# Performance work log

Hardware: AMD Instinct MI355X
Metric: run time of the kernel (lower is better)

## Reference

```python
import jax, jax.numpy as jnp
import numpy as np

N, E = 20000, 320000
H = 4            # heads per layer
C_IN, C_HID, C_OUT = 128, 64, 64
NEG_SLOPE = 0.2  # PyG GATConv default leaky_relu slope


def setup_inputs() -> dict:
    key = jax.random.key(0)
    ks = jax.random.split(key, 16)
    p = lambda k, shape: jax.random.normal(k, shape, jnp.float32) * 0.1
    return {
        "x": jax.random.normal(ks[0], (N, C_IN), jnp.float32),
        "edge_index": jax.random.randint(ks[1], (2, E), 0, N),
        # layer 0: in C_IN -> H*C_HID (concat)
        "W0": p(ks[2], (C_IN, H * C_HID)),
        "as0": p(ks[3], (H, C_HID)),
        "ad0": p(ks[4], (H, C_HID)),
        "b0": jnp.zeros((H * C_HID,), jnp.float32),
        # layer 1: in H*C_HID -> H*C_HID (concat)
        "W1": p(ks[5], (H * C_HID, H * C_HID)),
        "as1": p(ks[6], (H, C_HID)),
        "ad1": p(ks[7], (H, C_HID)),
        "b1": jnp.zeros((H * C_HID,), jnp.float32),
        # output layer: in H*C_HID -> C_OUT (mean over heads, concat=False)
        "W2": p(ks[8], (H * C_HID, H * C_OUT)),
        "as2": p(ks[9], (H, C_OUT)),
        "ad2": p(ks[10], (H, C_OUT)),
        "b2": jnp.zeros((C_OUT,), jnp.float32),
    }


def _gat_layer(x, src, dst, W, a_src, a_dst, b, concat):
    """PyG GATConv (eval mode): gather -> edge attention -> segment softmax -> scatter."""
    n = x.shape[0]
    h = (x @ W).reshape(n, H, -1)                      # [N, H, C]
    e_src = (h * a_src).sum(-1)                        # [N, H]
    e_dst = (h * a_dst).sum(-1)                        # [N, H]
    logits = jax.nn.leaky_relu(e_src[src] + e_dst[dst], NEG_SLOPE)   # [E', H]
    m = jax.lax.stop_gradient(jax.ops.segment_max(logits, dst, num_segments=n))
    ex = jnp.exp(logits - m[dst])
    denom = jax.ops.segment_sum(ex, dst, num_segments=n)
    alpha = ex / denom[dst]                            # [E', H] segment softmax per dst node
    out = jax.ops.segment_sum(h[src] * alpha[:, :, None], dst, num_segments=n)  # [N, H, C]
    out = out.reshape(n, -1) if concat else out.mean(axis=1)
    return out + b, alpha


def reference(x, edge_index, W0, as0, ad0, b0, W1, as1, ad1, b1, W2, as2, ad2, b2):
    n = x.shape[0]
    loops = jnp.arange(n, dtype=edge_index.dtype)      # GATConv adds self-loops
    src = jnp.concatenate([edge_index[0], loops])
    dst = jnp.concatenate([edge_index[1], loops])
    h, a0 = _gat_layer(x, src, dst, W0, as0, ad0, b0, True)
    h = jax.nn.elu(h)
    h, a1 = _gat_layer(h, src, dst, W1, as1, ad1, b1, True)
    h = jax.nn.elu(h)
    out, a2 = _gat_layer(h, src, dst, W2, as2, ad2, b2, False)
    return out, a0, a1, a2
```

## Files before the change

kernel.cpp:

```cpp
#include <hip/hip_runtime.h>
#include <hip/hip_bf16.h>
#include <math.h>

#define HCOLS 256
#define NHEAD 4
#define CDIM  64
#define NEG_SLOPE 0.2f

typedef __attribute__((ext_vector_type(8))) short bf16x8;
typedef __attribute__((ext_vector_type(4))) float f32x4;

__device__ __forceinline__ float leaky(float v) { return v > 0.f ? v : v * NEG_SLOPE; }
__device__ __forceinline__ float readlane_f(float v, int l) {
    return __uint_as_float(__builtin_amdgcn_readlane(__float_as_uint(v), l));
}
__device__ __forceinline__ unsigned short f2bf(float f) {
    unsigned u = __float_as_uint(f);
    u += 0x7fff + ((u >> 16) & 1);
    return (unsigned short)(u >> 16);
}
__device__ __forceinline__ float bf2f(unsigned short b) {
    return __uint_as_float(((unsigned)b) << 16);
}

__global__ void deg_kernel(const int* __restrict__ ei, int* __restrict__ deg,
                           int E, int Ep) {
    int e = blockIdx.x * 256 + threadIdx.x;
    if (e >= Ep) return;
    int d = (e < E) ? ei[E + e] : (e - E);
    atomicAdd(&deg[d], 1);
}

__global__ void scan_kernel(const int* __restrict__ deg, int* __restrict__ rowptr,
                            int* __restrict__ cursor, int n) {
    __shared__ int tmp[1024];
    __shared__ int carry_s;
    int tid = threadIdx.x;
    if (tid == 0) carry_s = 0;
    __syncthreads();
    for (int base = 0; base < n; base += 1024) {
        int i = base + tid;
        int v = (i < n) ? deg[i] : 0;
        tmp[tid] = v;
        __syncthreads();
        for (int off = 1; off < 1024; off <<= 1) {
            int t = (tid >= off) ? tmp[tid - off] : 0;
            __syncthreads();
            tmp[tid] += t;
            __syncthreads();
        }
        int excl = carry_s + tmp[tid] - v;
        if (i < n) { rowptr[i] = excl; cursor[i] = excl; }
        __syncthreads();
        if (tid == 1023) carry_s += tmp[1023];
        __syncthreads();
    }
    if (tid == 0) rowptr[n] = carry_s;
}

__global__ void fill_kernel(const int* __restrict__ ei, int* __restrict__ cursor,
                            int* __restrict__ eidx, int E, int Ep) {
    int e = blockIdx.x * 256 + threadIdx.x;
    if (e >= Ep) return;
    int d = (e < E) ? ei[E + e] : (e - E);
    int pos = atomicAdd(&cursor[d], 1);
    eidx[pos] = e;
}

__global__ void wconv_kernel(const float* __restrict__ W, unsigned short* __restrict__ Wt, int K) {
    __shared__ float t[32][33];
    int bx = blockIdx.x;
    int by = blockIdx.y;
    int tx = threadIdx.x & 31, ty = threadIdx.x >> 5;
#pragma unroll
    for (int i = 0; i < 32; i += 8)
        t[ty + i][tx] = W[(by * 32 + ty + i) * HCOLS + bx * 32 + tx];
    __syncthreads();
#pragma unroll
    for (int i = 0; i < 32; i += 8)
        Wt[(size_t)(bx * 32 + ty + i) * K + by * 32 + tx] = f2bf(t[tx][ty + i]);
}

template <int K, bool SRC_F32>
__global__ void gemm_kernel(const void* __restrict__ Xv, const unsigned short* __restrict__ Wt,
                            unsigned short* __restrict__ Hout,
                            const float* __restrict__ As, const float* __restrict__ Ad,
                            float* __restrict__ esrc, float* __restrict__ edst,
                            int n) {
    constexpr int LDK = K + 16;
    __shared__ __align__(16) unsigned short a_sh[32 * LDK];
    int row0 = blockIdx.x * 32;
    int tid = threadIdx.x;

    constexpr int CH = 32 * K / 8;
    for (int c = tid; c < CH; c += 256) {
        int r = c / (K / 8), kc = c % (K / 8);
        int row = row0 + r;
        uint4 pack;
        if (row < n) {
            if (SRC_F32) {
                const float* X = (const float*)Xv;
                float4 f0 = *reinterpret_cast<const float4*>(&X[(size_t)row * K + kc * 8]);
                float4 f1 = *reinterpret_cast<const float4*>(&X[(size_t)row * K + kc * 8 + 4]);
                pack.x = f2bf(f0.x) | ((unsigned)f2bf(f0.y) << 16);
                pack.y = f2bf(f0.z) | ((unsigned)f2bf(f0.w) << 16);
                pack.z = f2bf(f1.x) | ((unsigned)f2bf(f1.y) << 16);
                pack.w = f2bf(f1.z) | ((unsigned)f2bf(f1.w) << 16);
            } else {
                const uint4* X = (const uint4*)Xv;
                pack = X[((size_t)row * K + kc * 8) / 8];
            }
        } else {
            pack = make_uint4(0, 0, 0, 0);
        }
        *reinterpret_cast<uint4*>(&a_sh[r * LDK + kc * 8]) = pack;
    }
    __syncthreads();

    int lane = tid & 63;
    int w = tid >> 6;
    int lr = lane & 15;
    int lk = (lane >> 4) * 8;

    f32x4 acc[2][4];
#pragma unroll
    for (int m = 0; m < 2; ++m)
#pragma unroll
        for (int nf = 0; nf < 4; ++nf) acc[m][nf] = (f32x4){0.f, 0.f, 0.f, 0.f};

    const unsigned short* wt = Wt + (size_t)(w * 64) * K;
#pragma unroll
    for (int ks = 0; ks < K / 32; ++ks) {
        bf16x8 a[2], b[4];
#pragma unroll
        for (int m = 0; m < 2; ++m)
            a[m] = *reinterpret_cast<const bf16x8*>(&a_sh[(16 * m + lr) * LDK + ks * 32 + lk]);
#pragma unroll
        for (int nf = 0; nf < 4; ++nf)
            b[nf] = *reinterpret_cast<const bf16x8*>(&wt[(size_t)(16 * nf + lr) * K + ks * 32 + lk]);
#pragma unroll
        for (int m = 0; m < 2; ++m)
#pragma unroll
            for (int nf = 0; nf < 4; ++nf)
                acc[m][nf] = __builtin_amdgcn_mfma_f32_16x16x32_bf16(a[m], b[nf], acc[m][nf], 0, 0, 0);
    }

    float as_v[4], ad_v[4];
#pragma unroll
    for (int nf = 0; nf < 4; ++nf) {
        as_v[nf] = As[w * 64 + 16 * nf + lr];
        ad_v[nf] = Ad[w * 64 + 16 * nf + lr];
    }
#pragma unroll
    for (int m = 0; m < 2; ++m) {
#pragma unroll
        for (int j = 0; j < 4; ++j) {
            int row_g = row0 + 16 * m + (lane >> 4) * 4 + j;
            bool ok = row_g < n;
#pragma unroll
            for (int nf = 0; nf < 4; ++nf) {
                if (ok) Hout[(size_t)row_g * HCOLS + w * 64 + 16 * nf + lr] = f2bf(acc[m][nf][j]);
            }
            float ps = acc[m][0][j] * as_v[0] + acc[m][1][j] * as_v[1] +
                       acc[m][2][j] * as_v[2] + acc[m][3][j] * as_v[3];
            float pd = acc[m][0][j] * ad_v[0] + acc[m][1][j] * ad_v[1] +
                       acc[m][2][j] * ad_v[2] + acc[m][3][j] * ad_v[3];
#pragma unroll
            for (int off = 1; off < 16; off <<= 1) {
                ps += __shfl_xor(ps, off, 64);
                pd += __shfl_xor(pd, off, 64);
            }
            if (lr == 0 && ok) {
                esrc[row_g * NHEAD + w] = ps;
                edst[row_g * NHEAD + w] = pd;
            }
        }
    }
}

template <int MODE>
__global__ void attn_agg_kernel(const unsigned short* __restrict__ h,
                                const float* __restrict__ esrc,
                                const float* __restrict__ edst,
                                const int* __restrict__ ei,
                                const int* __restrict__ rowptr,
                                const int* __restrict__ eidx,
                                const float* __restrict__ bias,
                                float* __restrict__ alpha,
                                void* __restrict__ xout,
                                int n, int E) {
    int wave = threadIdx.x >> 6;
    int lane = threadIdx.x & 63;
    int node = blockIdx.x * 4 + wave;
    if (node >= n) return;
    int s0 = rowptr[node], s1 = rowptr[node + 1];
    int deg = s1 - s0;
    float4 ed = *reinterpret_cast<const float4*>(&edst[node * NHEAD]);

    int i0 = s0 + lane;
    bool valid = i0 < s1;
    int e0 = 0, sv = 0;
    float4 lg0 = make_float4(-3.4e38f, -3.4e38f, -3.4e38f, -3.4e38f);
    if (valid) {
        e0 = eidx[i0];
        sv = (e0 < E) ? ei[e0] : (e0 - E);
        float4 es = *reinterpret_cast<const float4*>(&esrc[sv * NHEAD]);
        lg0.x = leaky(es.x + ed.x);
        lg0.y = leaky(es.y + ed.y);
        lg0.z = leaky(es.z + ed.z);
        lg0.w = leaky(es.w + ed.w);
    }
    float4 mx = lg0;
    for (int i = i0 + 64; i < s1; i += 64) {
        int e = eidx[i];
        int s = (e < E) ? ei[e] : (e - E);
        float4 es = *reinterpret_cast<const float4*>(&esrc[s * NHEAD]);
        mx.x = fmaxf(mx.x, leaky(es.x + ed.x));
        mx.y = fmaxf(mx.y, leaky(es.y + ed.y));
        mx.z = fmaxf(mx.z, leaky(es.z + ed.z));
        mx.w = fmaxf(mx.w, leaky(es.w + ed.w));
    }
#pragma unroll
    for (int off = 32; off; off >>= 1) {
        mx.x = fmaxf(mx.x, __shfl_xor(mx.x, off, 64));
        mx.y = fmaxf(mx.y, __shfl_xor(mx.y, off, 64));
        mx.z = fmaxf(mx.z, __shfl_xor(mx.z, off, 64));
        mx.w = fmaxf(mx.w, __shfl_xor(mx.w, off, 64));
    }
    float4 ex0 = make_float4(0.f, 0.f, 0.f, 0.f);
    if (valid) {
        ex0.x = __expf(lg0.x - mx.x);
        ex0.y = __expf(lg0.y - mx.y);
        ex0.z = __expf(lg0.z - mx.z);
        ex0.w = __expf(lg0.w - mx.w);
    }
    float4 sm = ex0;
    for (int i = i0 + 64; i < s1; i += 64) {
        int e = eidx[i];
        int s = (e < E) ? ei[e] : (e - E);
        float4 es = *reinterpret_cast<const float4*>(&esrc[s * NHEAD]);
        sm.x += __expf(leaky(es.x + ed.x) - mx.x);
        sm.y += __expf(leaky(es.y + ed.y) - mx.y);
        sm.z += __expf(leaky(es.z + ed.z) - mx.z);
        sm.w += __expf(leaky(es.w + ed.w) - mx.w);
    }
#pragma unroll
    for (int off = 32; off; off >>= 1) {
        sm.x += __shfl_xor(sm.x, off, 64);
        sm.y += __shfl_xor(sm.y, off, 64);
        sm.z += __shfl_xor(sm.z, off, 64);
        sm.w += __shfl_xor(sm.w, off, 64);
    }
    float4 inv = make_float4(1.f / sm.x, 1.f / sm.y, 1.f / sm.z, 1.f / sm.w);
    float4 al = make_float4(ex0.x * inv.x, ex0.y * inv.y, ex0.z * inv.z, ex0.w * inv.w);
    if (valid) *reinterpret_cast<float4*>(&alpha[(size_t)e0 * NHEAD]) = al;
    for (int i = i0 + 64; i < s1; i += 64) {
        int e = eidx[i];
        int s = (e < E) ? ei[e] : (e - E);
        float4 es = *reinterpret_cast<const float4*>(&esrc[s * NHEAD]);
        float4 av;
        av.x = __expf(leaky(es.x + ed.x) - mx.x) * inv.x;
        av.y = __expf(leaky(es.y + ed.y) - mx.y) * inv.y;
        av.z = __expf(leaky(es.z + ed.z) - mx.z) * inv.z;
        av.w = __expf(leaky(es.w + ed.w) - mx.w) * inv.w;
        *reinterpret_cast<float4*>(&alpha[(size_t)e * NHEAD]) = av;
    }
    bool big = deg > 64;
    if (big) __threadfence();

    int head = lane >> 4;
    float4 acc = make_float4(0.f, 0.f, 0.f, 0.f);
    int m = deg < 64 ? deg : 64;
    for (int j = 0; j < m; ++j) {
        int s = __builtin_amdgcn_readlane(sv, j);
        float a0v = readlane_f(al.x, j);
        float a1v = readlane_f(al.y, j);
        float a2v = readlane_f(al.z, j);
        float a3v = readlane_f(al.w, j);
        float a = (head & 2) ? ((head & 1) ? a3v : a2v) : ((head & 1) ? a1v : a0v);
        ushort4 hv = *reinterpret_cast<const ushort4*>(&h[(size_t)s * HCOLS + (lane << 2)]);
        acc.x = fmaf(a, bf2f(hv.x), acc.x);
        acc.y = fmaf(a, bf2f(hv.y), acc.y);
        acc.z = fmaf(a, bf2f(hv.z), acc.z);
        acc.w = fmaf(a, bf2f(hv.w), acc.w);
    }
    if (big) {
        for (int i = s0 + 64; i < s1; ++i) {
            int e = eidx[i];
            int s = (e < E) ? ei[e] : (e - E);
            float4 av = *reinterpret_cast<const float4*>(&alpha[(size_t)e * NHEAD]);
            float a = (head & 2) ? ((head & 1) ? av.w : av.z) : ((head & 1) ? av.y : av.x);
            ushort4 hv = *reinterpret_cast<const ushort4*>(&h[(size_t)s * HCOLS + (lane << 2)]);
            acc.x = fmaf(a, bf2f(hv.x), acc.x);
            acc.y = fmaf(a, bf2f(hv.y), acc.y);
            acc.z = fmaf(a, bf2f(hv.z), acc.z);
            acc.w = fmaf(a, bf2f(hv.w), acc.w);
        }
    }
    if (MODE == 0) {
        float4 bv = *reinterpret_cast<const float4*>(&bias[lane << 2]);
        float4 v;
        v.x = acc.x + bv.x; v.y = acc.y + bv.y; v.z = acc.z + bv.z; v.w = acc.w + bv.w;
        v.x = v.x > 0.f ? v.x : expm1f(v.x);
        v.y = v.y > 0.f ? v.y : expm1f(v.y);
        v.z = v.z > 0.f ? v.z : expm1f(v.z);
        v.w = v.w > 0.f ? v.w : expm1f(v.w);
        ushort4 o;
        o.x = f2bf(v.x); o.y = f2bf(v.y); o.z = f2bf(v.z); o.w = f2bf(v.w);
        *reinterpret_cast<ushort4*>(&((unsigned short*)xout)[(size_t)node * HCOLS + (lane << 2)]) = o;
    } else {
        acc.x += __shfl_xor(acc.x, 16, 64); acc.x += __shfl_xor(acc.x, 32, 64);
        acc.y += __shfl_xor(acc.y, 16, 64); acc.y += __shfl_xor(acc.y, 32, 64);
        acc.z += __shfl_xor(acc.z, 16, 64); acc.z += __shfl_xor(acc.z, 32, 64);
        acc.w += __shfl_xor(acc.w, 16, 64); acc.w += __shfl_xor(acc.w, 32, 64);
        if (lane < 16) {
            float4 bv = *reinterpret_cast<const float4*>(&bias[lane << 2]);
            float4 v;
            v.x = acc.x * 0.25f + bv.x;
            v.y = acc.y * 0.25f + bv.y;
            v.z = acc.z * 0.25f + bv.z;
            v.w = acc.w * 0.25f + bv.w;
            *reinterpret_cast<float4*>(&((float*)xout)[(size_t)node * CDIM + (lane << 2)]) = v;
        }
    }
}

extern "C" void kernel_launch(void* const* d_in, const int* in_sizes, int n_in,
                              void* d_out, int out_size, void* d_ws, size_t ws_size,
                              hipStream_t stream) {
    const float* x   = (const float*)d_in[0];
    const int*   ei  = (const int*)d_in[1];
    const float* W0  = (const float*)d_in[2];
    const float* as0 = (const float*)d_in[3];
    const float* ad0 = (const float*)d_in[4];
    const float* b0  = (const float*)d_in[5];
    const float* W1  = (const float*)d_in[6];
    const float* as1 = (const float*)d_in[7];
    const float* ad1 = (const float*)d_in[8];
    const float* b1  = (const float*)d_in[9];
    const float* W2  = (const float*)d_in[10];
    const float* as2 = (const float*)d_in[11];
    const float* ad2 = (const float*)d_in[12];
    const float* b2  = (const float*)d_in[13];

    const int N  = in_sizes[0] / 128;
    const int E  = in_sizes[1] / 2;
    const int Ep = E + N;

    float* out = (float*)d_out;
    float* a0  = out + (size_t)N * CDIM;
    float* a1  = a0 + (size_t)Ep * NHEAD;
    float* a2  = a1 + (size_t)Ep * NHEAD;

    char* wp = (char*)d_ws;
    auto carve = [&](size_t bytes) {
        char* p = wp;
        wp += (bytes + 255) & ~(size_t)255;
        return (void*)p;
    };
    unsigned short* hbuf = (unsigned short*)carve((size_t)N * HCOLS * 2);
    unsigned short* xbuf = (unsigned short*)carve((size_t)N * HCOLS * 2);
    float* esrc   = (float*)carve((size_t)N * NHEAD * 4);
    float* edst   = (float*)carve((size_t)N * NHEAD * 4);
    int*   deg    = (int*)carve((size_t)N * 4);
    int*   rowptr = (int*)carve((size_t)(N + 1) * 4);
    int*   cursor = (int*)carve((size_t)N * 4);
    int*   eidx   = (int*)carve((size_t)Ep * 4);
    unsigned short* Wt0 = (unsigned short*)carve((size_t)HCOLS * 128 * 2);
    unsigned short* Wt1 = (unsigned short*)carve((size_t)HCOLS * HCOLS * 2);
    unsigned short* Wt2 = (unsigned short*)carve((size_t)HCOLS * HCOLS * 2);

    hipMemsetAsync(deg, 0, (size_t)N * 4, stream);
    deg_kernel<<<(Ep + 255) / 256, 256, 0, stream>>>(ei, deg, E, Ep);
    scan_kernel<<<1, 1024, 0, stream>>>(deg, rowptr, cursor, N);
    fill_kernel<<<(Ep + 255) / 256, 256, 0, stream>>>(ei, cursor, eidx, E, Ep);

    wconv_kernel<<<dim3(8, 4), 256, 0, stream>>>(W0, Wt0, 128);
    wconv_kernel<<<dim3(8, 8), 256, 0, stream>>>(W1, Wt1, 256);
    wconv_kernel<<<dim3(8, 8), 256, 0, stream>>>(W2, Wt2, 256);

    int gemm_grid = (N + 31) / 32;
    int agg_grid  = (N + 3) / 4;

    gemm_kernel<128, true><<<gemm_grid, 256, 0, stream>>>(x, Wt0, hbuf, as0, ad0, esrc, edst, N);
    attn_agg_kernel<0><<<agg_grid, 256, 0, stream>>>(hbuf, esrc, edst, ei, rowptr, eidx, b0, a0, xbuf, N, E);

    gemm_kernel<256, false><<<gemm_grid, 256, 0, stream>>>(xbuf, Wt1, hbuf, as1, ad1, esrc, edst, N);
    attn_agg_kernel<0><<<agg_grid, 256, 0, stream>>>(hbuf, esrc, edst, ei, rowptr, eidx, b1, a1, xbuf, N, E);

    gemm_kernel<256, false><<<gemm_grid, 256, 0, stream>>>(xbuf, Wt2, hbuf, as2, ad2, esrc, edst, N);
    attn_agg_kernel<1><<<agg_grid, 256, 0, stream>>>(hbuf, esrc, edst, ei, rowptr, eidx, b2, a2, out, N, E);
}
```

Before: 270.8 us.

## Stage per-edge alphas in LDS and unroll gather by 4; rewrite scan with wave shuffles

The aggregation loop no longer broadcasts each neighbor's alpha and source index with five readlanes and a per-lane head select. Each wave now writes alphas (transposed by head) and source indices to LDS and reads them back as float4/int4, handling four neighbors per iteration so four independent h gathers are in flight. Padded entries get alpha 0 and source 0, which makes the round-up to a multiple of 4 safe at the cost of a few wasted loads. The single-block scan is replaced by a chunked per-thread sum plus wave-shuffle prefix, removing the many __syncthreads rounds of the old scan.

```diff
diff --git a/kernel.cpp b/kernel.cpp
--- a/kernel.cpp
+++ b/kernel.cpp
@@ -11,9 +11,6 @@
 typedef __attribute__((ext_vector_type(4))) float f32x4;
 
 __device__ __forceinline__ float leaky(float v) { return v > 0.f ? v : v * NEG_SLOPE; }
-__device__ __forceinline__ float readlane_f(float v, int l) {
-    return __uint_as_float(__builtin_amdgcn_readlane(__float_as_uint(v), l));
-}
 __device__ __forceinline__ unsigned short f2bf(float f) {
     unsigned u = __float_as_uint(f);
     u += 0x7fff + ((u >> 16) & 1);
@@ -33,29 +30,41 @@
 
 __global__ void scan_kernel(const int* __restrict__ deg, int* __restrict__ rowptr,
                             int* __restrict__ cursor, int n) {
-    __shared__ int tmp[1024];
-    __shared__ int carry_s;
+    __shared__ int wsum[16];
     int tid = threadIdx.x;
-    if (tid == 0) carry_s = 0;
+    int lane = tid & 63, w = tid >> 6;
+    int CH = (n + 1023) >> 10;
+    int base = tid * CH;
+    int s = 0;
+    for (int k = 0; k < CH; ++k) {
+        int i = base + k;
+        s += (i < n) ? deg[i] : 0;
+    }
+    int incl = s;
+#pragma unroll
+    for (int d = 1; d < 64; d <<= 1) {
+        int t = __shfl_up(incl, d, 64);
+        if (lane >= d) incl += t;
+    }
+    if (lane == 63) wsum[w] = incl;
     __syncthreads();
-    for (int base = 0; base < n; base += 1024) {
-        int i = base + tid;
-        int v = (i < n) ? deg[i] : 0;
-        tmp[tid] = v;
-        __syncthreads();
-        for (int off = 1; off < 1024; off <<= 1) {
-            int t = (tid >= off) ? tmp[tid - off] : 0;
-            __syncthreads();
-            tmp[tid] += t;
-            __syncthreads();
+    if (w == 0) {
+        int v = (lane < 16) ? wsum[lane] : 0;
+#pragma unroll
+        for (int d = 1; d < 16; d <<= 1) {
+            int t = __shfl_up(v, d, 64);
+            if (lane >= d) v += t;
         }
-        int excl = carry_s + tmp[tid] - v;
-        if (i < n) { rowptr[i] = excl; cursor[i] = excl; }
-        __syncthreads();
-        if (tid == 1023) carry_s += tmp[1023];
-        __syncthreads();
-    }
-    if (tid == 0) rowptr[n] = carry_s;
+        if (lane < 16) wsum[lane] = v;
+    }
+    __syncthreads();
+    int woff = (w == 0) ? 0 : wsum[w - 1];
+    int run = woff + incl - s;
+    for (int k = 0; k < CH; ++k) {
+        int i = base + k;
+        if (i < n) { rowptr[i] = run; cursor[i] = run; run += deg[i]; }
+    }
+    if (tid == 1023) rowptr[n] = run;
 }
 
 __global__ void fill_kernel(const int* __restrict__ ei, int* __restrict__ cursor,
@@ -189,6 +198,9 @@
                                 float* __restrict__ alpha,
                                 void* __restrict__ xout,
                                 int n, int E) {
+    __shared__ __align__(16) float aT[4][NHEAD][72];
+    __shared__ __align__(16) int   sArr[4][64];
+
     int wave = threadIdx.x >> 6;
     int lane = threadIdx.x & 63;
     int node = blockIdx.x * 4 + wave;
@@ -268,21 +280,45 @@
     bool big = deg > 64;
     if (big) __threadfence();
 
+    aT[wave][0][lane] = valid ? al.x : 0.f;
+    aT[wave][1][lane] = valid ? al.y : 0.f;
+    aT[wave][2][lane] = valid ? al.z : 0.f;
+    aT[wave][3][lane] = valid ? al.w : 0.f;
+    sArr[wave][lane] = valid ? sv : 0;
+    asm volatile("s_waitcnt lgkmcnt(0)" ::: "memory");
+    __builtin_amdgcn_sched_barrier(0);
+
     int head = lane >> 4;
+    unsigned laneoff = (unsigned)(lane << 3);
+    const char* hb = (const char*)h;
     float4 acc = make_float4(0.f, 0.f, 0.f, 0.f);
     int m = deg < 64 ? deg : 64;
-    for (int j = 0; j < m; ++j) {
-        int s = __builtin_amdgcn_readlane(sv, j);
-        float a0v = readlane_f(al.x, j);
-        float a1v = readlane_f(al.y, j);
-        float a2v = readlane_f(al.z, j);
-        float a3v = readlane_f(al.w, j);
-        float a = (head & 2) ? ((head & 1) ? a3v : a2v) : ((head & 1) ? a1v : a0v);
-        ushort4 hv = *reinterpret_cast<const ushort4*>(&h[(size_t)s * HCOLS + (lane << 2)]);
-        acc.x = fmaf(a, bf2f(hv.x), acc.x);
-        acc.y = fmaf(a, bf2f(hv.y), acc.y);
-        acc.z = fmaf(a, bf2f(hv.z), acc.z);
-        acc.w = fmaf(a, bf2f(hv.w), acc.w);
+    int m4 = (m + 3) & ~3;
+    const float* aTp = &aT[wave][head][0];
+    const int*   sp  = &sArr[wave][0];
+    for (int j = 0; j < m4; j += 4) {
+        float4 a4 = *reinterpret_cast<const float4*>(aTp + j);
+        int4   s4 = *reinterpret_cast<const int4*>(sp + j);
+        uint2 h0 = *reinterpret_cast<const uint2*>(hb + (((unsigned)s4.x << 9) + laneoff));
+        uint2 h1 = *reinterpret_cast<const uint2*>(hb + (((unsigned)s4.y << 9) + laneoff));
+        uint2 h2 = *reinterpret_cast<const uint2*>(hb + (((unsigned)s4.z << 9) + laneoff));
+        uint2 h3 = *reinterpret_cast<const uint2*>(hb + (((unsigned)s4.w << 9) + laneoff));
+        acc.x = fmaf(a4.x, bf2f((unsigned short)(h0.x & 0xffff)), acc.x);
+        acc.y = fmaf(a4.x, bf2f((unsigned short)(h0.x >> 16)),    acc.y);
+        acc.z = fmaf(a4.x, bf2f((unsigned short)(h0.y & 0xffff)), acc.z);
+        acc.w = fmaf(a4.x, bf2f((unsigned short)(h0.y >> 16)),    acc.w);
+        acc.x = fmaf(a4.y, bf2f((unsigned short)(h1.x & 0xffff)), acc.x);
+        acc.y = fmaf(a4.y, bf2f((unsigned short)(h1.x >> 16)),    acc.y);
+        acc.z = fmaf(a4.y, bf2f((unsigned short)(h1.y & 0xffff)), acc.z);
+        acc.w = fmaf(a4.y, bf2f((unsigned short)(h1.y >> 16)),    acc.w);
+        acc.x = fmaf(a4.z, bf2f((unsigned short)(h2.x & 0xffff)), acc.x);
+        acc.y = fmaf(a4.z, bf2f((unsigned short)(h2.x >> 16)),    acc.y);
+        acc.z = fmaf(a4.z, bf2f((unsigned short)(h2.y & 0xffff)), acc.z);
+        acc.w = fmaf(a4.z, bf2f((unsigned short)(h2.y >> 16)),    acc.w);
+        acc.x = fmaf(a4.w, bf2f((unsigned short)(h3.x & 0xffff)), acc.x);
+        acc.y = fmaf(a4.w, bf2f((unsigned short)(h3.x >> 16)),    acc.y);
+        acc.z = fmaf(a4.w, bf2f((unsigned short)(h3.y & 0xffff)), acc.z);
+        acc.w = fmaf(a4.w, bf2f((unsigned short)(h3.y >> 16)),    acc.w);
     }
     if (big) {
         for (int i = s0 + 64; i < s1; ++i) {
@@ -290,11 +326,11 @@
             int s = (e < E) ? ei[e] : (e - E);
             float4 av = *reinterpret_cast<const float4*>(&alpha[(size_t)e * NHEAD]);
             float a = (head & 2) ? ((head & 1) ? av.w : av.z) : ((head & 1) ? av.y : av.x);
-            ushort4 hv = *reinterpret_cast<const ushort4*>(&h[(size_t)s * HCOLS + (lane << 2)]);
-            acc.x = fmaf(a, bf2f(hv.x), acc.x);
-            acc.y = fmaf(a, bf2f(hv.y), acc.y);
-            acc.z = fmaf(a, bf2f(hv.z), acc.z);
-            acc.w = fmaf(a, bf2f(hv.w), acc.w);
+            uint2 hv = *reinterpret_cast<const uint2*>(hb + (((unsigned)s << 9) + laneoff));
+            acc.x = fmaf(a, bf2f((unsigned short)(hv.x & 0xffff)), acc.x);
+            acc.y = fmaf(a, bf2f((unsigned short)(hv.x >> 16)),    acc.y);
+            acc.z = fmaf(a, bf2f((unsigned short)(hv.y & 0xffff)), acc.z);
+            acc.w = fmaf(a, bf2f((unsigned short)(hv.y >> 16)),    acc.w);
         }
     }
     if (MODE == 0) {
```

Result: faster. 244.1 us (-9.9%).
